# Kernel tuning notes

Hardware: AMD Instinct MI355X
Metric: run time of the kernel (lower is better)

Reference implementation:

```python
import jax, jax.numpy as jnp
import numpy as np

N, D, C = 50000, 128, 64
E = 800000
IN_DIM = 3 * D
EPS = 1e-8
TINY = 1e-12


def _manifold_point(key, n, d, hyperbolic):
    # expmap0 of a random tangent vector at origin o = e0 (ambient dim d)
    v = 0.3 * jax.random.normal(key, (n, d - 1), dtype=jnp.float32)
    nv = jnp.linalg.norm(v, axis=-1, keepdims=True)
    u = v / jnp.maximum(nv, TINY)
    if hyperbolic:  # Lorentz hyperboloid: (cosh|v|, sinh|v| u)
        return jnp.concatenate([jnp.cosh(nv), jnp.sinh(nv) * u], axis=-1)
    else:           # unit sphere: (cos|v|, sin|v| u)
        return jnp.concatenate([jnp.cos(nv), jnp.sin(nv) * u], axis=-1)


def logmap0_lorentz(x):
    # tangent at origin: first coord 0, spatial part = arccosh(x0) * x_r/|x_r|
    x0 = x[..., :1]
    xr = x[..., 1:]
    nr = jnp.linalg.norm(xr, axis=-1, keepdims=True)
    dist = jnp.arccosh(jnp.maximum(x0, 1.0))
    return jnp.concatenate([jnp.zeros_like(x0), dist * xr / jnp.maximum(nr, TINY)], axis=-1)


def logmap0_sphere(x):
    x0 = x[..., :1]
    xr = x[..., 1:]
    nr = jnp.linalg.norm(xr, axis=-1, keepdims=True)
    theta = jnp.arccos(jnp.clip(x0, -1.0, 1.0))
    return jnp.concatenate([jnp.zeros_like(x0), theta * xr / jnp.maximum(nr, TINY)], axis=-1)


def gcn_conv(x, edge_index, W, b, n):
    # PyG GCNConv: add self-loops, symmetric normalization D^-1/2 (A+I) D^-1/2 (X W) + b
    loops = jnp.arange(n, dtype=edge_index.dtype)
    src = jnp.concatenate([edge_index[0], loops])
    dst = jnp.concatenate([edge_index[1], loops])
    deg = jax.ops.segment_sum(jnp.ones_like(dst, dtype=x.dtype), dst, num_segments=n)
    dinv = jnp.where(deg > 0, deg ** -0.5, 0.0)
    norm = dinv[src] * dinv[dst]                 # [E+N]
    h = x @ W                                    # [N, cls_dim]
    msg = h[src] * norm[:, None]                 # [E+N, cls_dim]
    return jax.ops.segment_sum(msg, dst, num_segments=n) + b


def setup_inputs() -> dict:
    key = jax.random.key(0)
    k = jax.random.split(key, 7)
    x_E = jax.random.normal(k[0], (N, D), dtype=jnp.float32)
    x_H = _manifold_point(k[1], N, D, hyperbolic=True)
    x_S = _manifold_point(k[2], N, D, hyperbolic=False)
    edge_index = jax.random.randint(k[3], (2, E), 0, N, dtype=jnp.int64)
    W = jax.random.normal(k[4], (IN_DIM, D), dtype=jnp.float32) / np.sqrt(IN_DIM)
    b = jnp.zeros((D,), dtype=jnp.float32)
    cls_emb = jax.random.normal(k[5], (C, D), dtype=jnp.float32)
    return {"x_E": x_E, "x_H": x_H, "x_S": x_S, "edge_index": edge_index,
            "W": W, "b": b, "cls_emb": cls_emb}


def reference(x_E, x_H, x_S, edge_index, W, b, cls_emb):
    x_h = logmap0_lorentz(x_H)
    x_s = logmap0_sphere(x_S)
    x = jnp.concatenate([x_E, x_h, x_s], axis=-1)          # [N, 3D]
    x = gcn_conv(x, edge_index, W, b, N)                   # [N, D]
    # broadcast cosine similarity (torch eps=1e-8 semantics)
    xn = x / jnp.maximum(jnp.linalg.norm(x, axis=-1, keepdims=True), EPS)
    cn = cls_emb / jnp.maximum(jnp.linalg.norm(cls_emb, axis=-1, keepdims=True), EPS)
    return xn @ cn.T                                       # [N, C]
```

## Files before the change

kernel.cpp:

```cpp
#include <hip/hip_runtime.h>
#include <hip/hip_fp16.h>
#include <math.h>

#define NN 50000
#define DD 128
#define CC 64
#define EE 800000
#define IND 384
#define MAXDEG 64
#define CSTRIDE 16

typedef __attribute__((ext_vector_type(8))) _Float16 h8v;
typedef __attribute__((ext_vector_type(4))) float f4v;

static __device__ __forceinline__ unsigned short f2h(float f) {
  _Float16 h = (_Float16)f;
  return *reinterpret_cast<unsigned short*>(&h);
}
static __device__ __forceinline__ float h2f(unsigned short u) {
  _Float16 h = *reinterpret_cast<_Float16*>(&u);
  return (float)h;
}
static __device__ __forceinline__ float hlo(unsigned int u) {
  return h2f((unsigned short)(u & 0xffffu));
}
static __device__ __forceinline__ float hhi(unsigned int u) {
  return h2f((unsigned short)(u >> 16));
}

#define SCAL_B 12500
#define WT_B 192
__global__ __launch_bounds__(256) void k_prep2(const float* __restrict__ W,
                                               const float* __restrict__ cls,
                                               const float* __restrict__ xH,
                                               const float* __restrict__ xS,
                                               unsigned short* __restrict__ Wt,
                                               unsigned int* __restrict__ clsp,
                                               float* __restrict__ ch,
                                               float* __restrict__ cs,
                                               int4* __restrict__ cnt4, int n4) {
  int bid = blockIdx.x;
  int tid = threadIdx.x;
  if (bid < SCAL_B) {
    int gw = bid * 4 + (tid >> 6);
    int lane = tid & 63;
    const float2* h2 = (const float2*)(xH) + (size_t)gw * 64;
    float2 vh = h2[lane];
    float ssh = vh.x * vh.x + vh.y * vh.y;
    if (lane == 0) ssh -= vh.x * vh.x;
#pragma unroll
    for (int off = 32; off; off >>= 1) ssh += __shfl_down(ssh, off);
    const float2* s2 = (const float2*)(xS) + (size_t)gw * 64;
    float2 vs = s2[lane];
    float sss = vs.x * vs.x + vs.y * vs.y;
    if (lane == 0) sss -= vs.x * vs.x;
#pragma unroll
    for (int off = 32; off; off >>= 1) sss += __shfl_down(sss, off);
    if (lane == 0) {
      float nrh = sqrtf(ssh);
      float dist = acoshf(fmaxf(vh.x, 1.0f));
      ch[gw] = dist / fmaxf(nrh, 1e-12f);
      float nrs = sqrtf(sss);
      float th = acosf(fminf(fmaxf(vs.x, -1.0f), 1.0f));
      cs[gw] = th / fmaxf(nrs, 1e-12f);
    }
  } else if (bid < SCAL_B + WT_B) {
    int flat = (bid - SCAL_B) * 256 + tid;
    int n = flat / IND;
    int k = flat - n * IND;
    Wt[(size_t)n * IND + k] = f2h(W[(size_t)k * DD + n]);
  } else if (bid == SCAL_B + WT_B) {
    int wave = tid >> 6, lane = tid & 63;
    for (int c = wave; c < CC; c += 4) {
      const float2* r2 = (const float2*)(cls + (size_t)c * DD);
      float2 v = r2[lane];
      float ss = v.x * v.x + v.y * v.y;
#pragma unroll
      for (int off = 32; off; off >>= 1) ss += __shfl_xor(ss, off);
      float inv = 1.0f / fmaxf(sqrtf(ss), 1e-8f);
      clsp[c * 64 + lane] =
          (unsigned int)f2h(v.x * inv) | ((unsigned int)f2h(v.y * inv) << 16);
    }
  } else {
    int i = (bid - (SCAL_B + WT_B + 1)) * 256 + tid;
    if (i < n4) cnt4[i] = make_int4(0, 0, 0, 0);
  }
}

#define C_B 3125
#define G_B 1563
#define MEGA_B (C_B + G_B + 1)
__global__ __launch_bounds__(256) void k_mega(const int* __restrict__ esrc,
                                              const int* __restrict__ edst,
                                              int* __restrict__ cnt,
                                              unsigned short* __restrict__ col2,
                                              const float* __restrict__ xE,
                                              const float* __restrict__ xH,
                                              const float* __restrict__ xS,
                                              const float* __restrict__ sc1,
                                              const float* __restrict__ sc2,
                                              const unsigned short* __restrict__ Wt,
                                              unsigned short* __restrict__ h) {
  __shared__ unsigned short Ah[32 * 64];
  int bid = blockIdx.x;
  int tid = threadIdx.x;

  if (bid % 3 != 2) {
    int cid = (bid / 3) * 2 + (bid % 3);
    if (cid >= C_B) return;
    int e = cid * 256 + tid;
    int d = edst[e];
    int s = esrc[e];
    int slot = atomicAdd(&cnt[(size_t)d * CSTRIDE], 1);
    if (slot < MAXDEG) col2[(size_t)d * MAXDEG + slot] = (unsigned short)s;
    return;
  }

  int gid = bid / 3;
  int lane = tid & 63;
  int wid = tid >> 6;
  int c0 = wid * 32;
  int bm0 = gid * 32;
  int l15 = lane & 15;
  int lhi = lane >> 4;

  f4v acc[2][2];
#pragma unroll
  for (int m = 0; m < 2; ++m)
#pragma unroll
    for (int nf = 0; nf < 2; ++nf) acc[m][nf] = f4v{0.f, 0.f, 0.f, 0.f};

  for (int kb = 0; kb < IND; kb += 64) {
    int sec = kb >> 7;
    int off = kb & 127;
    const float* __restrict__ src = (sec == 0) ? xE : (sec == 1) ? xH : xS;
#pragma unroll
    for (int it = 0; it < 2; ++it) {
      int flat = tid + it * 256;
      int row = flat >> 4;
      int f4 = flat & 15;
      int node = bm0 + row;
      float4 v = make_float4(0.f, 0.f, 0.f, 0.f);
      float scale = 0.f;
      if (node < NN) {
        v = *(const float4*)&src[(size_t)node * DD + off + f4 * 4];
        scale = (sec == 0) ? 1.0f : (sec == 1) ? sc1[node] : sc2[node];
      }
      v.x *= scale; v.y *= scale; v.z *= scale; v.w *= scale;
      if (sec > 0 && off == 0 && f4 == 0) v.x = 0.f;
      ushort4 o;
      o.x = f2h(v.x); o.y = f2h(v.y); o.z = f2h(v.z); o.w = f2h(v.w);
      int idx = (row * 64 + f4 * 4) ^ ((row & 7) << 3);
      *(ushort4*)&Ah[idx] = o;
    }
    __syncthreads();
#pragma unroll
    for (int ks = 0; ks < 2; ++ks) {
      h8v a[2];
#pragma unroll
      for (int m = 0; m < 2; ++m) {
        int row = m * 16 + l15;
        int idx = (row * 64 + ks * 32 + lhi * 8) ^ ((row & 7) << 3);
        a[m] = *reinterpret_cast<const h8v*>(&Ah[idx]);
      }
      int kk = kb + ks * 32 + lhi * 8;
#pragma unroll
      for (int nf = 0; nf < 2; ++nf) {
        int n = c0 + nf * 16 + l15;
        h8v b = *reinterpret_cast<const h8v*>(&Wt[(size_t)n * IND + kk]);
#pragma unroll
        for (int m = 0; m < 2; ++m)
          acc[m][nf] = __builtin_amdgcn_mfma_f32_16x16x32_f16(a[m], b, acc[m][nf], 0, 0, 0);
      }
    }
    __syncthreads();
  }
#pragma unroll
  for (int m = 0; m < 2; ++m)
#pragma unroll
    for (int nf = 0; nf < 2; ++nf) {
      int colx = c0 + nf * 16 + l15;
      int rowb = bm0 + m * 16 + lhi * 4;
#pragma unroll
      for (int j = 0; j < 4; ++j) {
        int node = rowb + j;
        if (node < NN) h[(size_t)node * DD + colx] = f2h(acc[m][nf][j]);
      }
    }
}

__global__ __launch_bounds__(1024) void k_dfold(const int* __restrict__ cnt,
                                                float* __restrict__ dinv) {
  int i = blockIdx.x * 1024 + threadIdx.x;
  if (i < NN) dinv[i] = 1.0f / sqrtf((float)(cnt[(size_t)i * CSTRIDE] + 1));
}

__global__ __launch_bounds__(256) void k_aggout(const unsigned short* __restrict__ h,
                                                const int* __restrict__ cnt,
                                                const unsigned short* __restrict__ col2,
                                                const float* __restrict__ dinv,
                                                const float* __restrict__ b,
                                                const unsigned int* __restrict__ clsp,
                                                float* __restrict__ out) {
  __shared__ unsigned int xl[16 * 64];
  int tid = threadIdx.x;
  int li = tid & 15;
  int node16 = tid >> 4;
  int node = blockIdx.x * 16 + node16;

  const uint4* h4 = (const uint4*)h;
  float dv = dinv[node];
  uint4 hv = h4[(size_t)node * 16 + li];
  float a0 = dv * hlo(hv.x), a1 = dv * hhi(hv.x);
  float a2 = dv * hlo(hv.y), a3 = dv * hhi(hv.y);
  float a4 = dv * hlo(hv.z), a5 = dv * hhi(hv.z);
  float a6 = dv * hlo(hv.w), a7 = dv * hhi(hv.w);
  int ecnt = cnt[(size_t)node * CSTRIDE];
  if (ecnt > MAXDEG) ecnt = MAXDEG;
  const unsigned short* crow = col2 + (size_t)node * MAXDEG;
  int j = 0;
  for (; j + 15 < ecnt; j += 16) {
    int cc[16];
    float dd[16];
    uint4 vv[16];
#pragma unroll
    for (int q = 0; q < 16; ++q) cc[q] = crow[j + q];
#pragma unroll
    for (int q = 0; q < 16; ++q) dd[q] = dinv[cc[q]];
#pragma unroll
    for (int q = 0; q < 16; ++q) vv[q] = h4[(size_t)cc[q] * 16 + li];
#pragma unroll
    for (int q = 0; q < 16; ++q) {
      a0 += dd[q] * hlo(vv[q].x);
      a1 += dd[q] * hhi(vv[q].x);
      a2 += dd[q] * hlo(vv[q].y);
      a3 += dd[q] * hhi(vv[q].y);
      a4 += dd[q] * hlo(vv[q].z);
      a5 += dd[q] * hhi(vv[q].z);
      a6 += dd[q] * hlo(vv[q].w);
      a7 += dd[q] * hhi(vv[q].w);
    }
  }
  for (; j + 3 < ecnt; j += 4) {
    int c0_ = crow[j], c1_ = crow[j + 1], c2_ = crow[j + 2], c3_ = crow[j + 3];
    float d0 = dinv[c0_], d1 = dinv[c1_], d2 = dinv[c2_], d3 = dinv[c3_];
    uint4 v0 = h4[(size_t)c0_ * 16 + li];
    uint4 v1 = h4[(size_t)c1_ * 16 + li];
    uint4 v2 = h4[(size_t)c2_ * 16 + li];
    uint4 v3 = h4[(size_t)c3_ * 16 + li];
    a0 += d0 * hlo(v0.x) + d1 * hlo(v1.x) + d2 * hlo(v2.x) + d3 * hlo(v3.x);
    a1 += d0 * hhi(v0.x) + d1 * hhi(v1.x) + d2 * hhi(v2.x) + d3 * hhi(v3.x);
    a2 += d0 * hlo(v0.y) + d1 * hlo(v1.y) + d2 * hlo(v2.y) + d3 * hlo(v3.y);
    a3 += d0 * hhi(v0.y) + d1 * hhi(v1.y) + d2 * hhi(v2.y) + d3 * hhi(v3.y);
    a4 += d0 * hlo(v0.z) + d1 * hlo(v1.z) + d2 * hlo(v2.z) + d3 * hlo(v3.z);
    a5 += d0 * hhi(v0.z) + d1 * hhi(v1.z) + d2 * hhi(v2.z) + d3 * hhi(v3.z);
    a6 += d0 * hlo(v0.w) + d1 * hlo(v1.w) + d2 * hlo(v2.w) + d3 * hlo(v3.w);
    a7 += d0 * hhi(v0.w) + d1 * hhi(v1.w) + d2 * hhi(v2.w) + d3 * hhi(v3.w);
  }
  for (; j < ecnt; ++j) {
    int c_ = crow[j];
    float d_ = dinv[c_];
    uint4 v = h4[(size_t)c_ * 16 + li];
    a0 += d_ * hlo(v.x);
    a1 += d_ * hhi(v.x);
    a2 += d_ * hlo(v.y);
    a3 += d_ * hhi(v.y);
    a4 += d_ * hlo(v.z);
    a5 += d_ * hhi(v.z);
    a6 += d_ * hlo(v.w);
    a7 += d_ * hhi(v.w);
  }
  float4 b0 = ((const float4*)b)[li * 2];
  float4 b1 = ((const float4*)b)[li * 2 + 1];
  float r0 = dv * a0 + b0.x;
  float r1 = dv * a1 + b0.y;
  float r2 = dv * a2 + b0.z;
  float r3 = dv * a3 + b0.w;
  float r4 = dv * a4 + b1.x;
  float r5 = dv * a5 + b1.y;
  float r6 = dv * a6 + b1.z;
  float r7 = dv * a7 + b1.w;
  float ss = r0 * r0 + r1 * r1 + r2 * r2 + r3 * r3 +
             r4 * r4 + r5 * r5 + r6 * r6 + r7 * r7;
#pragma unroll
  for (int off = 8; off; off >>= 1) ss += __shfl_xor(ss, off);
  float inv = 1.0f / fmaxf(sqrtf(ss), 1e-8f);
  uint4 o;
  o.x = (unsigned int)f2h(r0 * inv) | ((unsigned int)f2h(r1 * inv) << 16);
  o.y = (unsigned int)f2h(r2 * inv) | ((unsigned int)f2h(r3 * inv) << 16);
  o.z = (unsigned int)f2h(r4 * inv) | ((unsigned int)f2h(r5 * inv) << 16);
  o.w = (unsigned int)f2h(r6 * inv) | ((unsigned int)f2h(r7 * inv) << 16);
  int widx = (node16 * 64 + li * 4) ^ ((node16 & 7) << 2);
  *(uint4*)&xl[widx] = o;
  __syncthreads();

  int lane = tid & 63;
  int wid = tid >> 6;
  int l15 = lane & 15, lhi = lane >> 4;
  f4v acc = f4v{0.f, 0.f, 0.f, 0.f};
  const uint4* clsp4 = (const uint4*)clsp;
#pragma unroll
  for (int ks = 0; ks < 4; ++ks) {
    int ridx = (l15 * 64 + ks * 16 + lhi * 4) ^ ((l15 & 7) << 2);
    h8v a = *reinterpret_cast<const h8v*>(&xl[ridx]);
    int n = wid * 16 + l15;
    uint4 bq = clsp4[n * 16 + ks * 4 + lhi];
    h8v bb = *reinterpret_cast<const h8v*>(&bq);
    acc = __builtin_amdgcn_mfma_f32_16x16x32_f16(a, bb, acc, 0, 0, 0);
  }
#pragma unroll
  for (int j2 = 0; j2 < 4; ++j2) {
    int nodeo = blockIdx.x * 16 + lhi * 4 + j2;
    out[(size_t)nodeo * CC + wid * 16 + l15] = acc[j2];
  }
}

extern "C" void kernel_launch(void* const* d_in, const int* in_sizes, int n_in,
                              void* d_out, int out_size, void* d_ws, size_t ws_size,
                              hipStream_t stream) {
  const float* xE = (const float*)d_in[0];
  const float* xH = (const float*)d_in[1];
  const float* xS = (const float*)d_in[2];
  const int* ei = (const int*)d_in[3];
  const float* W = (const float*)d_in[4];
  const float* b = (const float*)d_in[5];
  const float* cls = (const float*)d_in[6];
  float* out = (float*)d_out;

  char* ws = (char*)d_ws;
  size_t off = 0;
  auto alloc = [&](size_t bytes) {
    void* p = ws + off;
    off = (off + bytes + 255) & ~(size_t)255;
    return p;
  };
  unsigned short* h = (unsigned short*)alloc((size_t)NN * DD * 2);
  float* chv = (float*)alloc((size_t)NN * 4);
  float* csv = (float*)alloc((size_t)NN * 4);
  float* dinv = (float*)alloc((size_t)NN * 4);
  int* cnt = (int*)alloc((size_t)NN * CSTRIDE * 4);
  unsigned short* col2 = (unsigned short*)alloc((size_t)NN * MAXDEG * 2);
  unsigned short* Wt = (unsigned short*)alloc((size_t)DD * IND * 2);
  unsigned int* clsp = (unsigned int*)alloc((size_t)CC * 64 * 4);

  const int* esrc = ei;
  const int* edst = ei + EE;
  const int N4 = NN * CSTRIDE / 4;
  const int ZB = (N4 + 255) / 256;

  k_prep2<<<SCAL_B + WT_B + 1 + ZB, 256, 0, stream>>>(W, cls, xH, xS, Wt, clsp,
                                                      chv, csv, (int4*)cnt, N4);
  k_mega<<<MEGA_B, 256, 0, stream>>>(esrc, edst, cnt, col2, xE, xH, xS,
                                     chv, csv, Wt, h);
  k_dfold<<<(NN + 1023) / 1024, 1024, 0, stream>>>(cnt, dinv);
  k_aggout<<<NN / 16, 256, 0, stream>>>(h, cnt, col2, dinv, b, clsp, out);
}
```

Before: 129.1 us.

## Split edge bucketing across prep and GEMM kernels to balance work

Moves the zeroing of degree counters into its own small kernel. Half of the edge-bucketing atomics now run interleaved with the prep work (scalar logmap factors, W transpose, class normalisation) in a first fused kernel, and the other half run interleaved with the feature GEMM in the second kernel. The aim is to spread the latency-bound scatter atomics across two kernels so each overlaps with independent compute. In exchange it adds one extra kernel launch, and the edge order into the col2 buckets changes across the two kernels.

Measured after the change: 132.7 us. 1.03x slower.

```diff
diff --git a/kernel.cpp b/kernel.cpp
--- a/kernel.cpp
+++ b/kernel.cpp
@@ -9,6 +9,7 @@
 #define IND 384
 #define MAXDEG 64
 #define CSTRIDE 16
+#define E_SPLIT 400128
 
 typedef __attribute__((ext_vector_type(8))) _Float16 h8v;
 typedef __attribute__((ext_vector_type(4))) float f4v;
@@ -28,21 +29,49 @@
   return h2f((unsigned short)(u >> 16));
 }
 
+__global__ __launch_bounds__(256) void k_zero(int4* __restrict__ cnt4, int n4) {
+  int i = blockIdx.x * 256 + threadIdx.x;
+  if (i < n4) cnt4[i] = make_int4(0, 0, 0, 0);
+}
+
+#define C1_B 1563
 #define SCAL_B 12500
 #define WT_B 192
-__global__ __launch_bounds__(256) void k_prep2(const float* __restrict__ W,
+#define P_B (SCAL_B + WT_B + 1)
+#define MEGA1_B (C1_B + P_B)
+__global__ __launch_bounds__(256) void k_mega1(const int* __restrict__ esrc,
+                                               const int* __restrict__ edst,
+                                               int* __restrict__ cnt,
+                                               unsigned short* __restrict__ col2,
+                                               const float* __restrict__ W,
                                                const float* __restrict__ cls,
                                                const float* __restrict__ xH,
                                                const float* __restrict__ xS,
                                                unsigned short* __restrict__ Wt,
                                                unsigned int* __restrict__ clsp,
                                                float* __restrict__ ch,
-                                               float* __restrict__ cs,
-                                               int4* __restrict__ cnt4, int n4) {
+                                               float* __restrict__ cs) {
   int bid = blockIdx.x;
   int tid = threadIdx.x;
-  if (bid < SCAL_B) {
-    int gw = bid * 4 + (tid >> 6);
+  int cid = -1, pid = -1;
+  if (bid < 9 * C1_B) {
+    if (bid % 9 == 0) cid = bid / 9;
+    else pid = bid - bid / 9 - 1;
+  } else {
+    pid = bid - C1_B;
+  }
+
+  if (cid >= 0) {
+    int e = cid * 256 + tid;
+    int d = edst[e];
+    int s = esrc[e];
+    int slot = atomicAdd(&cnt[(size_t)d * CSTRIDE], 1);
+    if (slot < MAXDEG) col2[(size_t)d * MAXDEG + slot] = (unsigned short)s;
+    return;
+  }
+
+  if (pid < SCAL_B) {
+    int gw = pid * 4 + (tid >> 6);
     int lane = tid & 63;
     const float2* h2 = (const float2*)(xH) + (size_t)gw * 64;
     float2 vh = h2[lane];
@@ -64,12 +93,12 @@
       float th = acosf(fminf(fmaxf(vs.x, -1.0f), 1.0f));
       cs[gw] = th / fmaxf(nrs, 1e-12f);
     }
-  } else if (bid < SCAL_B + WT_B) {
-    int flat = (bid - SCAL_B) * 256 + tid;
+  } else if (pid < SCAL_B + WT_B) {
+    int flat = (pid - SCAL_B) * 256 + tid;
     int n = flat / IND;
     int k = flat - n * IND;
     Wt[(size_t)n * IND + k] = f2h(W[(size_t)k * DD + n]);
-  } else if (bid == SCAL_B + WT_B) {
+  } else {
     int wave = tid >> 6, lane = tid & 63;
     for (int c = wave; c < CC; c += 4) {
       const float2* r2 = (const float2*)(cls + (size_t)c * DD);
@@ -81,34 +110,32 @@
       clsp[c * 64 + lane] =
           (unsigned int)f2h(v.x * inv) | ((unsigned int)f2h(v.y * inv) << 16);
     }
-  } else {
-    int i = (bid - (SCAL_B + WT_B + 1)) * 256 + tid;
-    if (i < n4) cnt4[i] = make_int4(0, 0, 0, 0);
-  }
-}
-
-#define C_B 3125
+  }
+}
+
+#define C2_B 1562
 #define G_B 1563
-#define MEGA_B (C_B + G_B + 1)
-__global__ __launch_bounds__(256) void k_mega(const int* __restrict__ esrc,
-                                              const int* __restrict__ edst,
-                                              int* __restrict__ cnt,
-                                              unsigned short* __restrict__ col2,
-                                              const float* __restrict__ xE,
-                                              const float* __restrict__ xH,
-                                              const float* __restrict__ xS,
-                                              const float* __restrict__ sc1,
-                                              const float* __restrict__ sc2,
-                                              const unsigned short* __restrict__ Wt,
-                                              unsigned short* __restrict__ h) {
+#define MEGA2_B (C2_B + G_B + 2)
+__global__ __launch_bounds__(256) void k_mega2(const int* __restrict__ esrc,
+                                               const int* __restrict__ edst,
+                                               int* __restrict__ cnt,
+                                               unsigned short* __restrict__ col2,
+                                               const float* __restrict__ xE,
+                                               const float* __restrict__ xH,
+                                               const float* __restrict__ xS,
+                                               const float* __restrict__ sc1,
+                                               const float* __restrict__ sc2,
+                                               const unsigned short* __restrict__ Wt,
+                                               unsigned short* __restrict__ h) {
   __shared__ unsigned short Ah[32 * 64];
   int bid = blockIdx.x;
   int tid = threadIdx.x;
 
-  if (bid % 3 != 2) {
-    int cid = (bid / 3) * 2 + (bid % 3);
-    if (cid >= C_B) return;
-    int e = cid * 256 + tid;
+  if ((bid & 1) == 0) {
+    int cid = bid >> 1;
+    if (cid >= C2_B) return;
+    int e = E_SPLIT + cid * 256 + tid;
+    if (e >= EE) return;
     int d = edst[e];
     int s = esrc[e];
     int slot = atomicAdd(&cnt[(size_t)d * CSTRIDE], 1);
@@ -116,7 +143,8 @@
     return;
   }
 
-  int gid = bid / 3;
+  int gid = bid >> 1;
+  if (gid >= G_B) return;
   int lane = tid & 63;
   int wid = tid >> 6;
   int c0 = wid * 32;
@@ -346,12 +374,12 @@
   const int* esrc = ei;
   const int* edst = ei + EE;
   const int N4 = NN * CSTRIDE / 4;
-  const int ZB = (N4 + 255) / 256;
-
-  k_prep2<<<SCAL_B + WT_B + 1 + ZB, 256, 0, stream>>>(W, cls, xH, xS, Wt, clsp,
-                                                      chv, csv, (int4*)cnt, N4);
-  k_mega<<<MEGA_B, 256, 0, stream>>>(esrc, edst, cnt, col2, xE, xH, xS,
-                                     chv, csv, Wt, h);
+
+  k_zero<<<(N4 + 255) / 256, 256, 0, stream>>>((int4*)cnt, N4);
+  k_mega1<<<MEGA1_B, 256, 0, stream>>>(esrc, edst, cnt, col2, W, cls, xH, xS,
+                                       Wt, clsp, chv, csv);
+  k_mega2<<<MEGA2_B, 256, 0, stream>>>(esrc, edst, cnt, col2, xE, xH, xS,
+                                       chv, csv, Wt, h);
   k_dfold<<<(NN + 1023) / 1024, 1024, 0, stream>>>(cnt, dinv);
   k_aggout<<<NN / 16, 256, 0, stream>>>(h, cnt, col2, dinv, b, clsp, out);
 }
```
